# Kernel tuning notes

Hardware: AMD Instinct MI355X
Metric: run time of the kernel (lower is better)

## Reference

```python
import jax, jax.numpy as jnp
import numpy as np
from jax import lax

VOCAB, EMBED, HID, MID = 32000, 200, 10, 5
BSZ, SEQ = 256, 512
LN_EPS = 1e-5


def setup_inputs() -> dict:
    key = jax.random.key(0)
    ks = jax.random.split(key, 10)
    s = 0.1
    return {
        "src_tokens": jax.random.randint(ks[0], (BSZ, SEQ), 0, VOCAB, dtype=jnp.int64)
        if jax.config.jax_enable_x64 else jax.random.randint(ks[0], (BSZ, SEQ), 0, VOCAB, dtype=jnp.int32),
        "h0": jax.random.normal(ks[1], (1, BSZ, HID), jnp.float32),
        "c0": jax.random.normal(ks[2], (1, BSZ, HID), jnp.float32),
        "embed_W": jax.random.normal(ks[3], (VOCAB, EMBED), jnp.float32),
        "W_ih": jax.random.normal(ks[4], (4 * HID, EMBED), jnp.float32) * s,
        "W_hh": jax.random.normal(ks[5], (4 * HID, HID), jnp.float32) * s,
        "b_ih": jax.random.normal(ks[6], (4 * HID,), jnp.float32) * s,
        "b_hh": jax.random.normal(ks[7], (4 * HID,), jnp.float32) * s,
        "W1": jax.random.normal(ks[8], (MID, HID), jnp.float32) * s,
        "b1": jnp.zeros((MID,), jnp.float32),
        "ln_g": jnp.ones((MID,), jnp.float32),
        "ln_b": jnp.zeros((MID,), jnp.float32),
        "W2": jax.random.normal(ks[9], (1, MID), jnp.float32) * s,
        "b2": jnp.zeros((1,), jnp.float32),
    }


def reference(src_tokens, h0, c0, embed_W, W_ih, W_hh, b_ih, b_hh,
              W1, b1, ln_g, ln_b, W2, b2):
    # Embedding lookup -> [B, S, E] -> time-major [S, B, E]
    x = embed_W[src_tokens].astype(jnp.float32)
    x = jnp.transpose(x, (1, 0, 2))
    # Precompute input contribution to all 4 gates (i,f,g,o order, as torch)
    gates_x = jnp.einsum('sbe,ge->sbg', x, W_ih) + b_ih + b_hh  # [S, B, 4H]

    def step(carry, gx):
        h, c = carry
        gates = gx + h @ W_hh.T
        i, f, g, o = jnp.split(gates, 4, axis=-1)
        i = jax.nn.sigmoid(i)
        f = jax.nn.sigmoid(f)
        g = jnp.tanh(g)
        o = jax.nn.sigmoid(o)
        c = f * c + i * g
        h = o * jnp.tanh(c)
        return (h, c), None

    (hn, _), _ = lax.scan(step, (h0[0], c0[0]), gates_x)  # hn: [B, H]

    z = hn @ W1.T + b1  # [B, 5]
    mu = jnp.mean(z, axis=-1, keepdims=True)
    var = jnp.mean(jnp.square(z - mu), axis=-1, keepdims=True)
    z = (z - mu) * lax.rsqrt(var + LN_EPS) * ln_g + ln_b
    out = jax.nn.sigmoid(z @ W2.T + b2)  # [B, 1]
    return out[:, 0]  # squeeze -> [B]
```

## Files before the change

### kernel.cpp

```cpp
#include <hip/hip_runtime.h>
#include <math.h>

#define VOCAB 32000
#define EMBED 200
#define HID   10
#define GATES 40
#define BSZ   256
#define SEQ   512
#define PF    8

#define WROW3 44

__device__ __forceinline__ float rcp_fast(float x) { return __builtin_amdgcn_rcpf(x); }
__device__ __forceinline__ float exp2_fast(float x) { return __builtin_amdgcn_exp2f(x); }
__device__ __forceinline__ float readlane_f(float v, int l) {
    return __int_as_float(__builtin_amdgcn_readlane(__float_as_int(v), l));
}
template <int Q>
__device__ __forceinline__ float quad_bcast(float v) {
    return __int_as_float(__builtin_amdgcn_mov_dpp(
        __float_as_int(v), Q * 0x55, 0xF, 0xF, true));
}

#define SC_SIG (-1.442695041f)
#define SC_TNH (-2.885390082f)

__global__ __launch_bounds__(256) void proj_kernel(
    const float* __restrict__ embed, const float* __restrict__ Wih,
    const float* __restrict__ bih,   const float* __restrict__ bhh,
    float* __restrict__ proj)
{
    __shared__ float wT[EMBED * WROW3];
    const int tid = threadIdx.x;

    for (int idx = tid; idx < GATES * EMBED; idx += 256) {
        int g = idx / EMBED, k = idx - g * EMBED;
        wT[k * WROW3 + g] = Wih[idx];
    }
    __syncthreads();

    const int r  = blockIdx.x * 32 + (tid >> 3);
    const int li = tid & 7;
    const float* er = embed + (size_t)r * EMBED;

    float acc[GATES];
    #pragma unroll
    for (int g = 0; g < GATES; ++g) acc[g] = 0.f;

#define FMA40(K, EV) do {                                                   \
    const float* wr_ = &wT[(K) * WROW3];                                    \
    _Pragma("unroll")                                                       \
    for (int q = 0; q < 10; ++q) {                                          \
        float4 wv = *(const float4*)(wr_ + q * 4);                          \
        acc[4*q+0] = fmaf((EV), wv.x, acc[4*q+0]);                          \
        acc[4*q+1] = fmaf((EV), wv.y, acc[4*q+1]);                          \
        acc[4*q+2] = fmaf((EV), wv.z, acc[4*q+2]);                          \
        acc[4*q+3] = fmaf((EV), wv.w, acc[4*q+3]);                          \
    }                                                                       \
} while (0)

    #pragma unroll
    for (int c = 0; c < 6; ++c) {
        const int k0 = c * 32 + li * 4;
        float4 e = *(const float4*)(er + k0);
        FMA40(k0 + 0, e.x);
        FMA40(k0 + 1, e.y);
        FMA40(k0 + 2, e.z);
        FMA40(k0 + 3, e.w);
    }
    {
        const int k0 = 192 + li;
        float e = er[k0];
        FMA40(k0, e);
    }
#undef FMA40

    #pragma unroll
    for (int g = 0; g < GATES; ++g) {
        float v = acc[g];
        v += __shfl_xor(v, 1, 64);
        v += __shfl_xor(v, 2, 64);
        v += __shfl_xor(v, 4, 64);
        acc[g] = v;
    }

    const int g0 = li * 5;
    #pragma unroll
    for (int j = 0; j < 5; ++j) {
        int g = g0 + j;
        float sc = (g >= 20 && g < 30) ? SC_TNH : SC_SIG;
        proj[(size_t)r * GATES + g] = (acc[g] + bih[g] + bhh[g]) * sc;
    }
}

__global__ __launch_bounds__(64, 1) void lstm_rec(
    const int*   __restrict__ tok,  const float* __restrict__ proj,
    const float* __restrict__ h0,   const float* __restrict__ c0,
    const float* __restrict__ Whh,
    const float* __restrict__ W1,   const float* __restrict__ b1,
    const float* __restrict__ lng,  const float* __restrict__ lnb,
    const float* __restrict__ W2,   const float* __restrict__ b2,
    float* __restrict__ out)
{
    __shared__ int tok_s[SEQ + 2 * PF];

    const int b    = blockIdx.x;
    const int lane = threadIdx.x;
    const int j0   = min(lane >> 2, HID - 1);
    const int k4   = lane & 3;
    const int gate = k4 * HID + j0;

    #pragma unroll
    for (int k = 0; k < SEQ / 64; ++k)
        tok_s[k * 64 + lane] = tok[b * SEQ + k * 64 + lane];
    if (lane < 2 * PF) tok_s[SEQ + lane] = 0;
    __syncthreads();

    const float am  = (k4 == 2) ? 2.f : 1.f;
    const float amc = 1.f - am;
    const float amn = (k4 == 2) ? SC_TNH : SC_SIG;

    float w[HID];
    #pragma unroll
    for (int j = 0; j < HID; ++j) w[j] = amn * Whh[gate * HID + j];

    float hs[HID];
    #pragma unroll
    for (int u = 0; u < HID; ++u) hs[u] = h0[b * HID + u];
    float c_own = c0[b * HID + j0];

    int   tk_cur[PF], tk_nxt[PF];
    float gx_cur[PF], gx_nxt[PF];
    #pragma unroll
    for (int k = 0; k < PF; ++k) tk_cur[k] = tok_s[k];
    #pragma unroll
    for (int k = 0; k < PF; ++k) gx_cur[k] = proj[tk_cur[k] * GATES + gate];
    #pragma unroll
    for (int k = 0; k < PF; ++k) tk_nxt[k] = tok_s[PF + k];

    for (int s0 = 0; s0 < SEQ; s0 += PF) {
        #pragma unroll
        for (int k = 0; k < PF; ++k)
            gx_nxt[k] = proj[tk_nxt[k] * GATES + gate];
        #pragma unroll
        for (int k = 0; k < PF; ++k)
            tk_cur[k] = tok_s[s0 + 2 * PF + k];

        #pragma unroll
        for (int k = 0; k < PF; ++k) {
            float a0 = gx_cur[k], a1 = 0.f, a2 = 0.f, a3 = 0.f;
            a0 = fmaf(hs[0], w[0], a0); a1 = fmaf(hs[1], w[1], a1);
            a2 = fmaf(hs[2], w[2], a2); a3 = fmaf(hs[3], w[3], a3);
            a0 = fmaf(hs[4], w[4], a0); a1 = fmaf(hs[5], w[5], a1);
            a2 = fmaf(hs[6], w[6], a2); a3 = fmaf(hs[7], w[7], a3);
            a0 = fmaf(hs[8], w[8], a0); a1 = fmaf(hs[9], w[9], a1);
            float dt = (a0 + a2) + (a1 + a3);

            float t   = exp2_fast(dt);
            float sg  = rcp_fast(1.f + t);
            float val = fmaf(am, sg, amc);

            float iv = quad_bcast<0>(val);
            float fv = quad_bcast<1>(val);
            float gv = quad_bcast<2>(val);
            float ov = quad_bcast<3>(val);

            c_own = fmaf(fv, c_own, iv * gv);
            float t2 = exp2_fast(c_own * SC_TNH);
            float th = fmaf(2.f, rcp_fast(1.f + t2), -1.f);
            float h_own = ov * th;

            hs[0] = readlane_f(h_own, 0);  hs[1] = readlane_f(h_own, 4);
            hs[2] = readlane_f(h_own, 8);  hs[3] = readlane_f(h_own, 12);
            hs[4] = readlane_f(h_own, 16); hs[5] = readlane_f(h_own, 20);
            hs[6] = readlane_f(h_own, 24); hs[7] = readlane_f(h_own, 28);
            hs[8] = readlane_f(h_own, 32); hs[9] = readlane_f(h_own, 36);
        }

        #pragma unroll
        for (int k = 0; k < PF; ++k) {
            gx_cur[k] = gx_nxt[k];
            tk_nxt[k] = tk_cur[k];
        }
    }

    if (lane == 0) {
        float z[5];
        float mu = 0.f;
        #pragma unroll
        for (int m = 0; m < 5; ++m) {
            float a = b1[m];
            #pragma unroll
            for (int j = 0; j < HID; ++j) a = fmaf(hs[j], W1[m * HID + j], a);
            z[m] = a; mu += a;
        }
        mu *= 0.2f;
        float var = 0.f;
        #pragma unroll
        for (int m = 0; m < 5; ++m) { float d = z[m] - mu; var = fmaf(d, d, var); }
        var *= 0.2f;
        float rs = rsqrtf(var + 1e-5f);
        float acc = b2[0];
        #pragma unroll
        for (int m = 0; m < 5; ++m) {
            float zn = fmaf((z[m] - mu) * rs, lng[m], lnb[m]);
            acc = fmaf(zn, W2[m], acc);
        }
        out[b] = 1.f / (1.f + __expf(-acc));
    }
}

extern "C" void kernel_launch(void* const* d_in, const int* in_sizes, int n_in,
                              void* d_out, int out_size, void* d_ws, size_t ws_size,
                              hipStream_t stream) {
    const int*   tok   = (const int*)  d_in[0];
    const float* h0    = (const float*)d_in[1];
    const float* c0    = (const float*)d_in[2];
    const float* embed = (const float*)d_in[3];
    const float* Wih   = (const float*)d_in[4];
    const float* Whh   = (const float*)d_in[5];
    const float* bih   = (const float*)d_in[6];
    const float* bhh   = (const float*)d_in[7];
    const float* W1    = (const float*)d_in[8];
    const float* b1    = (const float*)d_in[9];
    const float* lng   = (const float*)d_in[10];
    const float* lnb   = (const float*)d_in[11];
    const float* W2    = (const float*)d_in[12];
    const float* b2    = (const float*)d_in[13];
    float* out  = (float*)d_out;
    float* proj = (float*)d_ws;

    hipLaunchKernelGGL(proj_kernel, dim3(VOCAB / 32), dim3(256), 0, stream,
                       embed, Wih, bih, bhh, proj);
    hipLaunchKernelGGL(lstm_rec, dim3(BSZ), dim3(64), 0, stream,
                       tok, proj, h0, c0, Whh, W1, b1, lng, lnb, W2, b2, out);
}
```

Before: 98.41 us.

## Restructure vocab projection to split embed dimension across waves with LDS reduction

The projection kernel now gives each thread one vocab row and one quarter of the embedding dimension. Each thread holds its embedding slice in registers and reads W_ih rows directly from global memory, which are uniform across the wave and so served from cache, instead of staging a transposed W_ih in LDS. The four partial sums are combined through shared memory. This removes the per-block LDS staging of W_ih and the cross-lane shuffles, at the cost of many global/scalar loads of W_ih per thread and higher register pressure from the 40 accumulators plus the embedding slice.

```diff
diff --git a/kernel.cpp b/kernel.cpp
--- a/kernel.cpp
+++ b/kernel.cpp
@@ -9,8 +9,6 @@
 #define SEQ   512
 #define PF    8
 
-#define WROW3 44
-
 __device__ __forceinline__ float rcp_fast(float x) { return __builtin_amdgcn_rcpf(x); }
 __device__ __forceinline__ float exp2_fast(float x) { return __builtin_amdgcn_exp2f(x); }
 __device__ __forceinline__ float readlane_f(float v, int l) {
@@ -24,72 +22,71 @@
 
 #define SC_SIG (-1.442695041f)
 #define SC_TNH (-2.885390082f)
+
+template <int NF4>
+__device__ __forceinline__ void dot_rows(
+    const float4* __restrict__ er,
+    const float*  __restrict__ wbase,
+    float* acc)
+{
+    float4 e4[NF4];
+    #pragma unroll
+    for (int i = 0; i < NF4; ++i) e4[i] = er[i];
+
+    for (int g = 0; g < GATES; ++g) {
+        const float4* wr = (const float4*)(wbase + g * EMBED);
+        float a0 = 0.f, a1 = 0.f, a2 = 0.f, a3 = 0.f;
+        #pragma unroll
+        for (int i = 0; i < NF4; ++i) {
+            float4 w4 = wr[i];
+            a0 = fmaf(e4[i].x, w4.x, a0);
+            a1 = fmaf(e4[i].y, w4.y, a1);
+            a2 = fmaf(e4[i].z, w4.z, a2);
+            a3 = fmaf(e4[i].w, w4.w, a3);
+        }
+        acc[g] = (a0 + a1) + (a2 + a3);
+    }
+}
 
 __global__ __launch_bounds__(256) void proj_kernel(
     const float* __restrict__ embed, const float* __restrict__ Wih,
     const float* __restrict__ bih,   const float* __restrict__ bhh,
     float* __restrict__ proj)
 {
-    __shared__ float wT[EMBED * WROW3];
+    __shared__ float red[3][64 * GATES];
+
     const int tid = threadIdx.x;
-
-    for (int idx = tid; idx < GATES * EMBED; idx += 256) {
-        int g = idx / EMBED, k = idx - g * EMBED;
-        wT[k * WROW3 + g] = Wih[idx];
+    const int r   = tid & 63;
+    const int kq  = tid >> 6;
+    const int row = blockIdx.x * 64 + r;
+    const float* erow = embed + (size_t)row * EMBED;
+
+    float acc[GATES];
+    if (kq == 0)      dot_rows<14>((const float4*)(erow +   0), Wih +   0, acc);
+    else if (kq == 1) dot_rows<12>((const float4*)(erow +  56), Wih +  56, acc);
+    else if (kq == 2) dot_rows<12>((const float4*)(erow + 104), Wih + 104, acc);
+    else              dot_rows<12>((const float4*)(erow + 152), Wih + 152, acc);
+
+    if (kq != 0) {
+        float* dst = &red[kq - 1][r * GATES];
+        #pragma unroll
+        for (int i = 0; i < GATES; ++i) dst[i] = acc[i];
     }
     __syncthreads();
 
-    const int r  = blockIdx.x * 32 + (tid >> 3);
-    const int li = tid & 7;
-    const float* er = embed + (size_t)r * EMBED;
-
-    float acc[GATES];
-    #pragma unroll
-    for (int g = 0; g < GATES; ++g) acc[g] = 0.f;
-
-#define FMA40(K, EV) do {                                                   \
-    const float* wr_ = &wT[(K) * WROW3];                                    \
-    _Pragma("unroll")                                                       \
-    for (int q = 0; q < 10; ++q) {                                          \
-        float4 wv = *(const float4*)(wr_ + q * 4);                          \
-        acc[4*q+0] = fmaf((EV), wv.x, acc[4*q+0]);                          \
-        acc[4*q+1] = fmaf((EV), wv.y, acc[4*q+1]);                          \
-        acc[4*q+2] = fmaf((EV), wv.z, acc[4*q+2]);                          \
-        acc[4*q+3] = fmaf((EV), wv.w, acc[4*q+3]);                          \
-    }                                                                       \
-} while (0)
-
-    #pragma unroll
-    for (int c = 0; c < 6; ++c) {
-        const int k0 = c * 32 + li * 4;
-        float4 e = *(const float4*)(er + k0);
-        FMA40(k0 + 0, e.x);
-        FMA40(k0 + 1, e.y);
-        FMA40(k0 + 2, e.z);
-        FMA40(k0 + 3, e.w);
-    }
-    {
-        const int k0 = 192 + li;
-        float e = er[k0];
-        FMA40(k0, e);
-    }
-#undef FMA40
-
-    #pragma unroll
-    for (int g = 0; g < GATES; ++g) {
-        float v = acc[g];
-        v += __shfl_xor(v, 1, 64);
-        v += __shfl_xor(v, 2, 64);
-        v += __shfl_xor(v, 4, 64);
-        acc[g] = v;
-    }
-
-    const int g0 = li * 5;
-    #pragma unroll
-    for (int j = 0; j < 5; ++j) {
-        int g = g0 + j;
-        float sc = (g >= 20 && g < 30) ? SC_TNH : SC_SIG;
-        proj[(size_t)r * GATES + g] = (acc[g] + bih[g] + bhh[g]) * sc;
+    if (kq == 0) {
+        #pragma unroll
+        for (int l = 0; l < 3; ++l) {
+            const float* src = &red[l][r * GATES];
+            #pragma unroll
+            for (int i = 0; i < GATES; ++i) acc[i] += src[i];
+        }
+        float* op = proj + (size_t)row * GATES;
+        #pragma unroll
+        for (int i = 0; i < GATES; ++i) {
+            float sc = (i >= 20 && i < 30) ? SC_TNH : SC_SIG;
+            op[i] = (acc[i] + bih[i] + bhh[i]) * sc;
+        }
     }
 }
 
@@ -230,7 +227,7 @@
     float* out  = (float*)d_out;
     float* proj = (float*)d_ws;
 
-    hipLaunchKernelGGL(proj_kernel, dim3(VOCAB / 32), dim3(256), 0, stream,
+    hipLaunchKernelGGL(proj_kernel, dim3(VOCAB / 64), dim3(256), 0, stream,
                        embed, Wih, bih, bhh, proj);
     hipLaunchKernelGGL(lstm_rec, dim3(BSZ), dim3(64), 0, stream,
                        tok, proj, h0, c0, Whh, W1, b1, lng, lnb, W2, b2, out);
```

New measurement: 99.10 us. About the same (+0.7%).
